# Optimization experiments

Measured on AMD Instinct MI355X. Metric: run time of the kernel, lower is better.

Reference implementation:

```python
import jax, jax.numpy as jnp
import numpy as np

B, C, W, H = 8, 256, 64, 64
C8 = C // 8


def setup_inputs() -> dict:
    key = jax.random.key(0)
    ks = jax.random.split(key, 8)
    # xavier_uniform for 1x1 convs: bound = sqrt(6/(fan_in+fan_out))
    def xavier(k, out_c, in_c):
        bound = np.sqrt(6.0 / (in_c + out_c))
        return jax.random.uniform(k, (out_c, in_c), jnp.float32, -bound, bound)
    return {
        "x": jax.random.normal(ks[0], (B, C, W, H), jnp.float32),
        "Wf": xavier(ks[1], C8, C),
        "bf": jnp.zeros((C8,), jnp.float32),
        "Wg": xavier(ks[2], C8, C),
        "bg": jnp.zeros((C8,), jnp.float32),
        "Wh": xavier(ks[3], C, C),
        "bh": jnp.zeros((C,), jnp.float32),
        "gamma": jnp.zeros((1,), jnp.float32),
    }


def reference(x, Wf, bf, Wg, bg, Wh, bh, gamma):
    b, c, w, h = x.shape
    n = w * h
    xf = x.reshape(b, c, n)                                   # (B, C, N)
    # 1x1 convs == per-position channel GEMMs
    f = jnp.einsum('oc,bcn->bon', Wf, xf) + bf[None, :, None]  # (B, C/8, N)
    g = jnp.einsum('oc,bcn->bon', Wg, xf) + bg[None, :, None]  # (B, C/8, N)
    hh = jnp.einsum('oc,bcn->bon', Wh, xf) + bh[None, :, None] # (B, C, N)
    # attention[b,i,j] = softmax_j( f[b,:,i] . g[b,:,j] )
    att = jax.nn.softmax(jnp.einsum('boi,boj->bij', f, g), axis=-1)
    # torch.bmm(h, attention): out[b,c,i] = sum_k h[b,c,k] * att[b,k,i]
    sa = jnp.einsum('bck,bki->bci', hh, att).reshape(b, c, w, h)
    return gamma * sa + x
```

## Files before the change

kernel.cpp:

```cpp
#include <hip/hip_runtime.h>
#include <hip/hip_bf16.h>

#define BB 8
#define CC 256
#define NN 4096
#define LOG2E 1.44269504088896340736f
#define SHIFT 48.0f

typedef __attribute__((ext_vector_type(8))) short short8;
typedef __attribute__((ext_vector_type(4))) float f32x4;

static __device__ __forceinline__ unsigned short f2b(float x) {
  __hip_bfloat16 h = __float2bfloat16(x);
  return *reinterpret_cast<unsigned short*>(&h);
}
static __device__ __forceinline__ unsigned int pk2(float a, float b) {
  return (unsigned int)f2b(a) | ((unsigned int)f2b(b) << 16);
}


__global__ __launch_bounds__(256) void k_wprep(
    const float* __restrict__ Wf, const float* __restrict__ bfv,
    const float* __restrict__ Wg, const float* __restrict__ bgv,
    const float* __restrict__ Wh, const float* __restrict__ bhv,
    unsigned short* __restrict__ wA, float* __restrict__ ball)
{
  const int t = threadIdx.x;
  const int fi = blockIdx.x * 4 + (t >> 6);
  const int l = t & 63;
  const int mg = fi >> 3, kg = fi & 7;
  const int o = mg * 16 + (l & 15);
  const int c0 = kg * 32 + (l >> 4) * 8;
  const float* src; float scale = 1.0f;
  if (o < 32)      { src = Wf + (size_t)o * CC; scale = LOG2E; }
  else if (o < 64) { src = Wg + (size_t)(o - 32) * CC; }
  else             { src = Wh + (size_t)(o - 64) * CC; }
  float4 a = *(const float4*)(src + c0);
  float4 c = *(const float4*)(src + c0 + 4);
  short8 v;
  v[0] = (short)f2b(a.x * scale); v[1] = (short)f2b(a.y * scale);
  v[2] = (short)f2b(a.z * scale); v[3] = (short)f2b(a.w * scale);
  v[4] = (short)f2b(c.x * scale); v[5] = (short)f2b(c.y * scale);
  v[6] = (short)f2b(c.z * scale); v[7] = (short)f2b(c.w * scale);
  *(short8*)(wA + (size_t)fi * 512 + l * 8) = v;
  if (blockIdx.x == 0 && t < 320)
    ball[t] = (t < 32) ? bfv[t] * LOG2E : (t < 64) ? bgv[t - 32] : bhv[t - 64];
}

__global__ __launch_bounds__(512) void k_fgh(
    const float* __restrict__ x, const unsigned short* __restrict__ wA,
    const float* __restrict__ ball,
    unsigned short* __restrict__ fA, unsigned short* __restrict__ gB,
    unsigned short* __restrict__ hA)
{
  __shared__ __align__(16) char smem[41984];
  unsigned short* xb = (unsigned short*)smem;
  unsigned short* TL = (unsigned short*)smem;
  const int bid = blockIdx.x;
  const int b = bid & 7, i0 = (bid >> 3) * 64;
  const int t = threadIdx.x, w = t >> 6, l = t & 63;
  const int ig_w = w & 3, mg0 = (w >> 2) * 10;
  f32x4 acc[10] = {};
  for (int cc = 0; cc < 4; ++cc) {
    __syncthreads();
    {
      short8 v;
      const float* xp = x + ((size_t)b * CC + cc * 64 + w * 8) * NN + i0 + l;
      #pragma unroll
      for (int e = 0; e < 8; ++e) v[e] = (short)f2b(xp[(size_t)e * NN]);
      int frag = (w >> 2) * 4 + (l >> 4);
      int lp = (w & 3) * 16 + (l & 15);
      *(short8*)(xb + (frag * 64 + lp) * 8) = v;
    }
    __syncthreads();
    #pragma unroll
    for (int kg2 = 0; kg2 < 2; ++kg2) {
      short8 bfrag = *(const short8*)(xb + ((kg2 * 4 + ig_w) * 64 + l) * 8);
      int kg = cc * 2 + kg2;
      #pragma unroll
      for (int j = 0; j < 10; ++j) {
        short8 afrag = *(const short8*)(wA +
            ((size_t)((mg0 + j) * 8 + kg)) * 512 + l * 8);
        acc[j] = __builtin_amdgcn_mfma_f32_16x16x32_bf16(afrag, bfrag, acc[j], 0, 0, 0);
      }
    }
  }
  __syncthreads();
  #pragma unroll
  for (int j = 0; j < 10; ++j) {
    int ob = (mg0 + j) * 16 + (l >> 4) * 4;
    float4 bl = *(const float4*)(ball + ob);
    int irow = ig_w * 16 + (l & 15);
    ushort4 pv;
    pv.x = f2b(acc[j][0] + bl.x); pv.y = f2b(acc[j][1] + bl.y);
    pv.z = f2b(acc[j][2] + bl.z); pv.w = f2b(acc[j][3] + bl.w);
    *(ushort4*)(TL + irow * 328 + ob) = pv;
  }
  __syncthreads();
  if (t < 256) {
    int kg_p = t >> 6;
    int o8 = (l >> 4) * 8;
    int irow = kg_p * 16 + (l & 15);
    short8 vf = *(const short8*)(TL + irow * 328 + o8);
    short8 vg = *(const short8*)(TL + irow * 328 + 32 + o8);
    size_t kgG = (size_t)b * 256 + (i0 >> 4) + kg_p;
    *(short8*)(fA + kgG * 512 + l * 8) = vf;
    *(short8*)(gB + kgG * 512 + l * 8) = vg;
  }
  #pragma unroll
  for (int q = 0; q < 4; ++q) {
    int slot = t + q * 512;
    int fr = slot >> 6, ll = slot & 63;
    int cg = fr >> 1, kcl = fr & 1;
    int orow = 64 + cg * 16 + (ll & 15);
    int pbase = kcl * 32 + (ll >> 4) * 8;
    short8 v;
    #pragma unroll
    for (int e = 0; e < 8; ++e) v[e] = (short)TL[(pbase + e) * 328 + orow];
    size_t idx = (((size_t)b * 16 + cg) * 128 + (i0 >> 5) + kcl) * 512 + ll * 8;
    *(short8*)(hA + idx) = v;
  }
}

__global__ __launch_bounds__(512) void k_stats(
    const unsigned short* __restrict__ fA, const unsigned short* __restrict__ gB,
    float* __restrict__ cshift)
{
  __shared__ __align__(16) unsigned short sg[2][16 * 512];
  const int bid = blockIdx.x;
  const int b = bid & 7, kt = bid >> 3;
  const int t = threadIdx.x, w = t >> 6, l = t & 63;
  const int li = l & 15, lh = l >> 4;
  short8 af = *(const short8*)(fA + ((size_t)b * 256 + kt * 8 + w) * 512 + l * 8);
  const unsigned short* gb = gB + (size_t)b * 256 * 512;
  f32x4 zero = {0.f, 0.f, 0.f, 0.f};
  {
    uint4 v0 = *(const uint4*)(gb + ((size_t)(w * 2 + 0) * 64 + l) * 8);
    uint4 v1 = *(const uint4*)(gb + ((size_t)(w * 2 + 1) * 64 + l) * 8);
    *(uint4*)(&sg[0][((w * 2 + 0) * 64 + l) * 8]) = v0;
    *(uint4*)(&sg[0][((w * 2 + 1) * 64 + l) * 8]) = v1;
  }
  __syncthreads();
  float s[4] = {0.f, 0.f, 0.f, 0.f};
  for (int jt = 0; jt < 16; ++jt) {
    if (jt < 15) {
      uint4 v0 = *(const uint4*)(gb + ((size_t)((jt + 1) * 16 + w * 2 + 0) * 64 + l) * 8);
      uint4 v1 = *(const uint4*)(gb + ((size_t)((jt + 1) * 16 + w * 2 + 1) * 64 + l) * 8);
      unsigned short* dst = &sg[(jt + 1) & 1][0];
      *(uint4*)(dst + ((w * 2 + 0) * 64 + l) * 8) = v0;
      *(uint4*)(dst + ((w * 2 + 1) * 64 + l) * 8) = v1;
    }
    const unsigned short* src = &sg[jt & 1][0];
    #pragma unroll
    for (int jf = 0; jf < 16; ++jf) {
      short8 bfrag = *(const short8*)(src + (jf * 64 + l) * 8);
      f32x4 d = __builtin_amdgcn_mfma_f32_16x16x32_bf16(af, bfrag, zero, 0, 0, 0);
      s[0] += exp2f(d[0] - SHIFT);
      s[1] += exp2f(d[1] - SHIFT);
      s[2] += exp2f(d[2] - SHIFT);
      s[3] += exp2f(d[3] - SHIFT);
    }
    __syncthreads();
  }
  #pragma unroll
  for (int mk = 1; mk < 16; mk <<= 1)
    #pragma unroll
    for (int r = 0; r < 4; ++r) s[r] += __shfl_xor(s[r], mk);
  if (li == 0) {
    #pragma unroll
    for (int r = 0; r < 4; ++r) {
      size_t idx = (size_t)b * NN + (kt * 8 + w) * 16 + lh * 4 + r;
      cshift[idx] = SHIFT + log2f(fmaxf(s[r], 1e-30f));
    }
  }
}

__global__ __launch_bounds__(256) void k_out(
    const unsigned short* __restrict__ fA, const unsigned short* __restrict__ gB,
    const unsigned short* __restrict__ hA,
    const float* __restrict__ csv,
    const float* __restrict__ x, const float* __restrict__ gamma,
    float* __restrict__ out)
{
  __shared__ __align__(16) unsigned short pbuf[2 * 8 * 512];
  const int bid = blockIdx.x;
  const int b = bid & 7, i0 = (bid >> 3) * 64;
  const int t = threadIdx.x, w = t >> 6, l = t & 63;
  const int li = l & 15, lh = l >> 4;
  const unsigned short* fAb = fA + (size_t)b * 256 * 512 + l * 8;
  const unsigned short* hAb = hA + ((size_t)b * 16 + w * 4) * (size_t)128 * 512 + l * 8;
  const float* cs = csv + (size_t)b * NN + w * 16 + lh * 4;
  short8 g[4];
  #pragma unroll
  for (int ig = 0; ig < 4; ++ig)
    g[ig] = *(const short8*)(gB + ((size_t)b * 256 + (i0 >> 4) + ig) * 512 + l * 8);
  const int lt = ((w & 1) * 2 + (lh >> 1)) * 16 + li;
  f32x4 zero = {0.f, 0.f, 0.f, 0.f};
  f32x4 acc[4][4] = {};
  short8 afc = *(const short8*)(fAb + (size_t)w * 512);
  float4 ccc = *(const float4*)(cs);
  for (int ch = 0; ch < 64; ++ch) {
    short8 hf[8];
    #pragma unroll
    for (int cgl = 0; cgl < 4; ++cgl)
      #pragma unroll
      for (int ks = 0; ks < 2; ++ks)
        hf[cgl * 2 + ks] = *(const short8*)(hAb +
            ((size_t)cgl * 128 + ch * 2 + ks) * 512);
    unsigned short* pb = pbuf + (ch & 1) * 4096;
    #pragma unroll
    for (int ig = 0; ig < 4; ++ig) {
      f32x4 s = __builtin_amdgcn_mfma_f32_16x16x32_bf16(afc, g[ig], zero, 0, 0, 0);
      uint2 v;
      v.x = pk2(exp2f(s[0] - ccc.x), exp2f(s[1] - ccc.y));
      v.y = pk2(exp2f(s[2] - ccc.z), exp2f(s[3] - ccc.w));
      *(uint2*)((char*)pb + (((w >> 1) * 4 + ig) * 64 + lt) * 16 + (lh & 1) * 8) = v;
    }
    if (ch < 63) {
      afc = *(const short8*)(fAb + (size_t)((ch + 1) * 4 + w) * 512);
      ccc = *(const float4*)(cs + (ch + 1) * 64);
    }
    __syncthreads();
    #pragma unroll
    for (int ks = 0; ks < 2; ++ks) {
      short8 pf[4];
      #pragma unroll
      for (int ig = 0; ig < 4; ++ig)
        pf[ig] = *(const short8*)(pb + ((ks * 4 + ig) * 64 + l) * 8);
      #pragma unroll
      for (int cgl = 0; cgl < 4; ++cgl)
        #pragma unroll
        for (int ig = 0; ig < 4; ++ig)
          acc[cgl][ig] = __builtin_amdgcn_mfma_f32_16x16x32_bf16(
              pf[ig], hf[cgl * 2 + ks], acc[cgl][ig], 0, 0, 0);
    }
  }
  const float gm = gamma[0];
  #pragma unroll
  for (int cgl = 0; cgl < 4; ++cgl)
    #pragma unroll
    for (int ig = 0; ig < 4; ++ig) {
      int c = (w * 4 + cgl) * 16 + li;
      int i = i0 + ig * 16 + lh * 4;
      size_t off = ((size_t)b * CC + c) * NN + i;
      float4 xv = *(const float4*)(x + off);
      float4 ov;
      ov.x = gm * acc[cgl][ig][0] + xv.x;
      ov.y = gm * acc[cgl][ig][1] + xv.y;
      ov.z = gm * acc[cgl][ig][2] + xv.z;
      ov.w = gm * acc[cgl][ig][3] + xv.w;
      *(float4*)(out + off) = ov;
    }
}

extern "C" void kernel_launch(void* const* d_in, const int* in_sizes, int n_in,
                              void* d_out, int out_size, void* d_ws, size_t ws_size,
                              hipStream_t stream)
{
  const float* x     = (const float*)d_in[0];
  const float* Wf    = (const float*)d_in[1];
  const float* bf    = (const float*)d_in[2];
  const float* Wg    = (const float*)d_in[3];
  const float* bg    = (const float*)d_in[4];
  const float* Wh    = (const float*)d_in[5];
  const float* bh    = (const float*)d_in[6];
  const float* gamma = (const float*)d_in[7];
  float* out = (float*)d_out;

  char* wsb = (char*)d_ws;
  float* cshift = (float*)(wsb + 131072);
  unsigned short* wA = (unsigned short*)(wsb + 262144);
  float* ball        = (float*)(wsb + 425984);
  unsigned short* fA = (unsigned short*)(wsb + 427520);
  unsigned short* gB = (unsigned short*)(wsb + 2524672);
  unsigned short* hA = (unsigned short*)(wsb + 4621824);

  k_wprep<<<40,  256, 0, stream>>>(Wf, bf, Wg, bg, Wh, bh, wA, ball);
  k_fgh  <<<512, 512, 0, stream>>>(x, wA, ball, fA, gB, hA);
  k_stats<<<256, 512, 0, stream>>>(fA, gB, cshift);
  k_out  <<<512, 256, 0, stream>>>(fA, gB, hA, cshift, x, gamma, out);
}
```

Measured before the change: 180.0 us.

## Use 32x32x16 MFMA in output kernel with 512-thread blocks and repacked h

Repacks the h operand into 32-row fragments and rewrites the attention-times-h accumulation to use 32x32x16 bf16 MFMA with two 16-float accumulators per wave. Blocks grow to 8 waves, each computing its own 16-key score slice, and each chunk now covers 128 keys instead of 64, so there are half as many barriers. The aim is to cut per-FLOP MFMA issue overhead and LDS operand reads. The trade-off is a larger LDS buffer, no prefetch of the next f and cshift chunk, and more register pressure under the launch-bounds occupancy hint.

```diff
diff --git a/kernel.cpp b/kernel.cpp
--- a/kernel.cpp
+++ b/kernel.cpp
@@ -9,6 +9,7 @@
 
 typedef __attribute__((ext_vector_type(8))) short short8;
 typedef __attribute__((ext_vector_type(4))) float f32x4;
+typedef __attribute__((ext_vector_type(16))) float f32x16;
 
 static __device__ __forceinline__ unsigned short f2b(float x) {
   __hip_bfloat16 h = __float2bfloat16(x);
@@ -111,13 +112,13 @@
   for (int q = 0; q < 4; ++q) {
     int slot = t + q * 512;
     int fr = slot >> 6, ll = slot & 63;
-    int cg = fr >> 1, kcl = fr & 1;
-    int orow = 64 + cg * 16 + (ll & 15);
-    int pbase = kcl * 32 + (ll >> 4) * 8;
+    int cg = fr >> 2, kcl = fr & 3;
+    int orow = 64 + cg * 32 + (ll & 31);
+    int pbase = kcl * 16 + (ll >> 5) * 8;
     short8 v;
     #pragma unroll
     for (int e = 0; e < 8; ++e) v[e] = (short)TL[(pbase + e) * 328 + orow];
-    size_t idx = (((size_t)b * 16 + cg) * 128 + (i0 >> 5) + kcl) * 512 + ll * 8;
+    size_t idx = (((size_t)b * 8 + cg) * 256 + (i0 >> 4) + kcl) * 512 + ll * 8;
     *(short8*)(hA + idx) = v;
   }
 }
@@ -175,82 +176,74 @@
   }
 }
 
-__global__ __launch_bounds__(256) void k_out(
+__global__ __launch_bounds__(512, 4) void k_out(
     const unsigned short* __restrict__ fA, const unsigned short* __restrict__ gB,
     const unsigned short* __restrict__ hA,
     const float* __restrict__ csv,
     const float* __restrict__ x, const float* __restrict__ gamma,
     float* __restrict__ out)
 {
-  __shared__ __align__(16) unsigned short pbuf[2 * 8 * 512];
+  __shared__ __align__(16) unsigned short pbuf[2 * 16 * 512];
   const int bid = blockIdx.x;
   const int b = bid & 7, i0 = (bid >> 3) * 64;
   const int t = threadIdx.x, w = t >> 6, l = t & 63;
   const int li = l & 15, lh = l >> 4;
-  const unsigned short* fAb = fA + (size_t)b * 256 * 512 + l * 8;
-  const unsigned short* hAb = hA + ((size_t)b * 16 + w * 4) * (size_t)128 * 512 + l * 8;
+  const unsigned short* fAb = fA + ((size_t)b * 256 + w) * 512 + l * 8;
+  const unsigned short* hAb = hA + ((size_t)b * 8 + w) * (size_t)256 * 512 + l * 8;
   const float* cs = csv + (size_t)b * NN + w * 16 + lh * 4;
   short8 g[4];
   #pragma unroll
   for (int ig = 0; ig < 4; ++ig)
     g[ig] = *(const short8*)(gB + ((size_t)b * 256 + (i0 >> 4) + ig) * 512 + l * 8);
-  const int lt = ((w & 1) * 2 + (lh >> 1)) * 16 + li;
+  const int ltb = (lh >> 1) * 32 + li;
+  const int eb2 = (lh & 1) * 8;
   f32x4 zero = {0.f, 0.f, 0.f, 0.f};
-  f32x4 acc[4][4] = {};
-  short8 afc = *(const short8*)(fAb + (size_t)w * 512);
-  float4 ccc = *(const float4*)(cs);
-  for (int ch = 0; ch < 64; ++ch) {
+  f32x16 acc0 = {0,0,0,0,0,0,0,0,0,0,0,0,0,0,0,0};
+  f32x16 acc1 = {0,0,0,0,0,0,0,0,0,0,0,0,0,0,0,0};
+  for (int ch = 0; ch < 32; ++ch) {
     short8 hf[8];
     #pragma unroll
-    for (int cgl = 0; cgl < 4; ++cgl)
-      #pragma unroll
-      for (int ks = 0; ks < 2; ++ks)
-        hf[cgl * 2 + ks] = *(const short8*)(hAb +
-            ((size_t)cgl * 128 + ch * 2 + ks) * 512);
-    unsigned short* pb = pbuf + (ch & 1) * 4096;
+    for (int ks = 0; ks < 8; ++ks)
+      hf[ks] = *(const short8*)(hAb + ((size_t)ch * 8 + ks) * 512);
+    short8 af = *(const short8*)(fAb + (size_t)ch * 8 * 512);
+    float4 cc = *(const float4*)(cs + ch * 128);
+    unsigned short* pb = pbuf + (ch & 1) * 8192;
     #pragma unroll
     for (int ig = 0; ig < 4; ++ig) {
-      f32x4 s = __builtin_amdgcn_mfma_f32_16x16x32_bf16(afc, g[ig], zero, 0, 0, 0);
+      f32x4 s = __builtin_amdgcn_mfma_f32_16x16x32_bf16(af, g[ig], zero, 0, 0, 0);
       uint2 v;
-      v.x = pk2(exp2f(s[0] - ccc.x), exp2f(s[1] - ccc.y));
-      v.y = pk2(exp2f(s[2] - ccc.z), exp2f(s[3] - ccc.w));
-      *(uint2*)((char*)pb + (((w >> 1) * 4 + ig) * 64 + lt) * 16 + (lh & 1) * 8) = v;
-    }
-    if (ch < 63) {
-      afc = *(const short8*)(fAb + (size_t)((ch + 1) * 4 + w) * 512);
-      ccc = *(const float4*)(cs + (ch + 1) * 64);
-    }
-    __syncthreads();
-    #pragma unroll
-    for (int ks = 0; ks < 2; ++ks) {
-      short8 pf[4];
-      #pragma unroll
-      for (int ig = 0; ig < 4; ++ig)
-        pf[ig] = *(const short8*)(pb + ((ks * 4 + ig) * 64 + l) * 8);
-      #pragma unroll
-      for (int cgl = 0; cgl < 4; ++cgl)
-        #pragma unroll
-        for (int ig = 0; ig < 4; ++ig)
-          acc[cgl][ig] = __builtin_amdgcn_mfma_f32_16x16x32_bf16(
-              pf[ig], hf[cgl * 2 + ks], acc[cgl][ig], 0, 0, 0);
+      v.x = pk2(exp2f(s[0] - cc.x), exp2f(s[1] - cc.y));
+      v.y = pk2(exp2f(s[2] - cc.z), exp2f(s[3] - cc.w));
+      *(uint2*)((char*)pb + (((ig >> 1) * 8 + w) * 64 + ltb + (ig & 1) * 16) * 16 + eb2) = v;
+    }
+    __syncthreads();
+    #pragma unroll
+    for (int ks = 0; ks < 8; ++ks) {
+      short8 pf0 = *(const short8*)(pb + ((0 * 8 + ks) * 64 + l) * 8);
+      short8 pf1 = *(const short8*)(pb + ((1 * 8 + ks) * 64 + l) * 8);
+      acc0 = __builtin_amdgcn_mfma_f32_32x32x16_bf16(pf0, hf[ks], acc0, 0, 0, 0);
+      acc1 = __builtin_amdgcn_mfma_f32_32x32x16_bf16(pf1, hf[ks], acc1, 0, 0, 0);
     }
   }
   const float gm = gamma[0];
-  #pragma unroll
-  for (int cgl = 0; cgl < 4; ++cgl)
-    #pragma unroll
-    for (int ig = 0; ig < 4; ++ig) {
-      int c = (w * 4 + cgl) * 16 + li;
-      int i = i0 + ig * 16 + lh * 4;
+  const int c = w * 32 + (l & 31);
+  const int l5 = (l >> 5) * 4;
+  #pragma unroll
+  for (int iF = 0; iF < 2; ++iF) {
+    const f32x16 accv = (iF == 0) ? acc0 : acc1;
+    #pragma unroll
+    for (int rq = 0; rq < 4; ++rq) {
+      int i = i0 + iF * 32 + rq * 8 + l5;
       size_t off = ((size_t)b * CC + c) * NN + i;
       float4 xv = *(const float4*)(x + off);
       float4 ov;
-      ov.x = gm * acc[cgl][ig][0] + xv.x;
-      ov.y = gm * acc[cgl][ig][1] + xv.y;
-      ov.z = gm * acc[cgl][ig][2] + xv.z;
-      ov.w = gm * acc[cgl][ig][3] + xv.w;
+      ov.x = gm * accv[rq * 4 + 0] + xv.x;
+      ov.y = gm * accv[rq * 4 + 1] + xv.y;
+      ov.z = gm * accv[rq * 4 + 2] + xv.z;
+      ov.w = gm * accv[rq * 4 + 3] + xv.w;
       *(float4*)(out + off) = ov;
     }
+  }
 }
 
 extern "C" void kernel_launch(void* const* d_in, const int* in_sizes, int n_in,
@@ -278,5 +271,5 @@
   k_wprep<<<40,  256, 0, stream>>>(Wf, bf, Wg, bg, Wh, bh, wA, ball);
   k_fgh  <<<512, 512, 0, stream>>>(x, wA, ball, fA, gB, hA);
   k_stats<<<256, 512, 0, stream>>>(fA, gB, cshift);
-  k_out  <<<512, 256, 0, stream>>>(fA, gB, hA, cshift, x, gamma, out);
-}
+  k_out  <<<512, 512, 0, stream>>>(fA, gB, hA, cshift, x, gamma, out);
+}
```

After: 168.4 us. 6.4% less time.
